# Optimization experiments

Measured on AMD Instinct MI355X. Metric: run time of the kernel, lower is better.

The kernel has to match this reference:

```python
import jax, jax.numpy as jnp
import numpy as np

N = 100000
E = 1600000
IN_FEATS = 256
HID = 128


def _graph_conv(x, W, b, src, dst, n_nodes):
    # DGL GraphConv with norm='both':
    #   out = D_in^{-1/2} * A * (D_out^{-1/2} * x @ W) + b
    ones = jnp.ones(src.shape[0], dtype=x.dtype)
    deg_out = jax.ops.segment_sum(ones, src, num_segments=n_nodes)
    deg_in = jax.ops.segment_sum(ones, dst, num_segments=n_nodes)
    norm_src = jnp.maximum(deg_out, 1.0) ** -0.5  # [N]
    norm_dst = jnp.maximum(deg_in, 1.0) ** -0.5   # [N]
    h = (x * norm_src[:, None]) @ W               # [N, HID]
    msg = h[src]                                  # [E, HID] gather
    agg = jax.ops.segment_sum(msg, dst, num_segments=n_nodes)  # [N, HID] scatter-add
    return agg * norm_dst[:, None] + b


def setup_inputs() -> dict:
    key = jax.random.key(0)
    ks = jax.random.split(key, 12)
    x = jax.random.normal(ks[0], (N, IN_FEATS), dtype=jnp.float32)
    src0 = jax.random.randint(ks[1], (E,), 0, N, dtype=jnp.int32)
    dst0 = jax.random.randint(ks[2], (E,), 0, N, dtype=jnp.int32)
    src1 = jax.random.randint(ks[3], (E,), 0, N, dtype=jnp.int32)
    dst1 = jax.random.randint(ks[4], (E,), 0, N, dtype=jnp.int32)
    s_e = 1.0 / np.sqrt(IN_FEATS)
    s_h = 1.0 / np.sqrt(HID)
    We = jax.random.uniform(ks[5], (IN_FEATS, HID), jnp.float32, -s_e, s_e)
    be = jax.random.uniform(ks[6], (HID,), jnp.float32, -s_e, s_e)
    W1 = jax.random.uniform(ks[7], (HID, HID), jnp.float32, -s_h, s_h)
    b1 = jnp.zeros((HID,), jnp.float32)
    W2 = jax.random.uniform(ks[8], (HID, HID), jnp.float32, -s_h, s_h)
    b2 = jnp.zeros((HID,), jnp.float32)
    return {"x": x, "We": We, "be": be, "W1": W1, "b1": b1, "W2": W2, "b2": b2,
            "src0": src0, "dst0": dst0, "src1": src1, "dst1": dst1}


def reference(x, We, be, W1, b1, W2, b2, src0, dst0, src1, dst1):
    n = x.shape[0]
    h = x @ We + be                                   # embed
    h = jax.nn.relu(_graph_conv(h, W1, b1, src0, dst0, n))
    h = jax.nn.relu(_graph_conv(h, W2, b2, src1, dst1, n))
    return h
```

## Files before the change

kernel.cpp:

```cpp
#include <hip/hip_runtime.h>

#define HID 128
#define NBUCK 512
#define BSHIFT 8
#define NB 512
#define M4 (4 * NBUCK * NB)
#define STAGE_CAP 8192

typedef __attribute__((ext_vector_type(8))) short bf16x8;
typedef __attribute__((ext_vector_type(4))) float f32x4;

__device__ __forceinline__ unsigned short f2bf(float f) {
    union { float f; unsigned u; } v; v.f = f;
    unsigned r = v.u + 0x7fff + ((v.u >> 16) & 1);
    return (unsigned short)(r >> 16);
}
__device__ __forceinline__ float bf2f(unsigned short b) {
    union { float f; unsigned u; } v; v.u = ((unsigned)b) << 16;
    return v.f;
}

__device__ __forceinline__ void gload_lds16(const void* g, void* l) {
    __builtin_amdgcn_global_load_lds(
        (const __attribute__((address_space(1))) void*)g,
        (__attribute__((address_space(3))) void*)l, 16, 0, 0);
}

__global__ __launch_bounds__(256) void bucket_count_all(
    const int* __restrict__ k0, const int* __restrict__ k1,
    const int* __restrict__ k2, const int* __restrict__ k3,
    int* __restrict__ counts, int E, int chunk) {
    __shared__ int h[4][NBUCK];
    int tid = threadIdx.x;
    #pragma unroll
    for (int j = 0; j < 8; ++j) ((int*)h)[tid + j * 256] = 0;
    __syncthreads();
    int base = blockIdx.x * chunk;
    int end = min(base + chunk, E);
    const int* keys[4] = {k0, k1, k2, k3};
    #pragma unroll
    for (int p = 0; p < 4; ++p) {
        const int* kp = keys[p];
        for (int i = base + tid; i < end; i += 256)
            atomicAdd(&h[p][kp[i] >> BSHIFT], 1);
    }
    __syncthreads();
    #pragma unroll
    for (int p = 0; p < 4; ++p) {
        counts[((p << 9) + tid) * NB + blockIdx.x] = h[p][tid];
        counts[((p << 9) + tid + 256) * NB + blockIdx.x] = h[p][tid + 256];
    }
}

__global__ __launch_bounds__(256) void scan_a(int* __restrict__ data, int* __restrict__ partials, int m) {
    __shared__ int sdata[256];
    int base = blockIdx.x * 1024;
    int tid = threadIdx.x;
    int v[4]; int s = 0;
    #pragma unroll
    for (int i = 0; i < 4; ++i) { int idx = base + tid * 4 + i; v[i] = (idx < m) ? data[idx] : 0; s += v[i]; }
    sdata[tid] = s; __syncthreads();
    for (int off = 1; off < 256; off <<= 1) {
        int t = (tid >= off) ? sdata[tid - off] : 0; __syncthreads();
        sdata[tid] += t; __syncthreads();
    }
    int excl = sdata[tid] - s;
    if (tid == 255) partials[blockIdx.x] = sdata[255];
    int run = excl;
    #pragma unroll
    for (int i = 0; i < 4; ++i) { int idx = base + tid * 4 + i; if (idx < m) data[idx] = run; run += v[i]; }
}

__global__ __launch_bounds__(1024) void scan_b(int* __restrict__ partials, int nb) {
    __shared__ int sdata[1024];
    int tid = threadIdx.x;
    int v = (tid < nb) ? partials[tid] : 0;
    sdata[tid] = v; __syncthreads();
    for (int off = 1; off < 1024; off <<= 1) {
        int t = (tid >= off) ? sdata[tid - off] : 0; __syncthreads();
        sdata[tid] += t; __syncthreads();
    }
    if (tid < nb) partials[tid] = sdata[tid] - v;
}

__global__ __launch_bounds__(256) void scan_c(int* __restrict__ data, const int* __restrict__ partials, int m) {
    int i = blockIdx.x * 256 + threadIdx.x;
    if (i < m) data[i] += partials[i >> 10];
}

__global__ __launch_bounds__(256) void bucket_scatter_all(
    const int* __restrict__ k0, const int* __restrict__ k1,
    const int* __restrict__ k2, const int* __restrict__ k3,
    const int* __restrict__ pay0, const int* __restrict__ pay1,
    const int* __restrict__ scanned, unsigned* __restrict__ bucketed,
    int E, int chunk) {
    __shared__ unsigned cur[4][NBUCK];
    int tid = threadIdx.x;
    int blk = blockIdx.x;
    #pragma unroll
    for (int p = 0; p < 4; ++p) {
        cur[p][tid]       = (unsigned)scanned[((p << 9) + tid) * NB + blk];
        cur[p][tid + 256] = (unsigned)scanned[((p << 9) + tid + 256) * NB + blk];
    }
    __syncthreads();
    int base = blk * chunk;
    int end = min(base + chunk, E);
    const int* keys[4] = {k0, k1, k2, k3};
    const int* pays[4] = {pay0, pay1, nullptr, nullptr};
    #pragma unroll
    for (int p = 0; p < 4; ++p) {
        const int* kp = keys[p];
        const int* pp = pays[p];
        for (int i = base + tid; i < end; i += 256) {
            int k = kp[i];
            int b = k >> BSHIFT;
            unsigned pay = pp ? (unsigned)pp[i] : 0u;
            unsigned pos = atomicAdd(&cur[p][b], 1u);
            bucketed[pos] = ((unsigned)(k & 255) << 17) | pay;
        }
    }
}

__global__ __launch_bounds__(256) void bucket_finalize(
    unsigned* __restrict__ bucketed, const int* __restrict__ scanned,
    int* __restrict__ rowptr0, int* __restrict__ rowptr1,
    int* __restrict__ dout0, int* __restrict__ dout1, int n, int E) {
    __shared__ unsigned stage[STAGE_CAP];
    __shared__ int cnt[256];
    __shared__ int sd[256];
    __shared__ int excl[256];
    __shared__ int cur[256];
    int tid = threadIdx.x;
    int g = blockIdx.x;
    int p = g >> 9;
    int b = g & 511;
    int start = scanned[g * NB];
    int end = (g == 4 * NBUCK - 1) ? 4 * E : scanned[(g + 1) * NB];
    if (end - start > STAGE_CAP) end = start + STAGE_CAP;
    int len = end - start;
    int node0 = b << BSHIFT;

    cnt[tid] = 0;
    __syncthreads();
    if (p < 2) {
        for (int i = tid; i < len; i += 256) {
            unsigned v = bucketed[start + i];
            stage[i] = v;
            atomicAdd(&cnt[v >> 17], 1);
        }
    } else {
        for (int i = tid; i < len; i += 256)
            atomicAdd(&cnt[bucketed[start + i] >> 17], 1);
    }
    __syncthreads();

    if (p >= 2) {
        int* dout = (p == 2) ? dout0 : dout1;
        int node = node0 + tid;
        if (node < n) dout[node] = cnt[tid];
        return;
    }

    int v = cnt[tid];
    sd[tid] = v;
    __syncthreads();
    for (int off = 1; off < 256; off <<= 1) {
        int t = (tid >= off) ? sd[tid - off] : 0; __syncthreads();
        sd[tid] += t; __syncthreads();
    }
    excl[tid] = sd[tid] - v;
    cur[tid] = 0;
    __syncthreads();

    int startLocal = start - p * E;
    int* rp = (p == 0) ? rowptr0 : rowptr1;
    int node = node0 + tid;
    if (node < n) rp[node] = startLocal + excl[tid];
    if (b == NBUCK - 1 && tid == 0) rp[n] = E;

    int* csr = (int*)bucketed + p * E;
    for (int i = tid; i < len; i += 256) {
        unsigned w = stage[i];
        int nl = (int)(w >> 17);
        int pos = startLocal + excl[nl] + atomicAdd(&cur[nl], 1);
        csr[pos] = (int)(w & 0x1FFFFu);
    }
}

__device__ __forceinline__ size_t bswz_idx(int k, int col) {
    int s = k >> 5, lh = (k >> 3) & 3, j = k & 7;
    int c = col >> 4, lc = col & 15;
    return ((((size_t)s * 8 + c) * 64 + (lh * 16 + lc)) * 8 + j);
}

__global__ __launch_bounds__(256) void weight_fuse(
    const float* __restrict__ We, const float* __restrict__ be,
    const float* __restrict__ W1,
    unsigned short* __restrict__ B1h, unsigned short* __restrict__ B1l,
    float* __restrict__ cv) {
    __shared__ float w1[128][128];
    int tid = threadIdx.x;
    #pragma unroll
    for (int it = 0; it < 16; ++it) {
        int s = tid + it * 256;
        int r = s >> 5, c4 = (s & 31) << 2;
        *(float4*)&w1[r][c4] = *(const float4*)&W1[r * 128 + c4];
    }
    __syncthreads();
    int j = tid & 127;
    int half = tid >> 7;
    if (blockIdx.x == 128) {
        if (half) return;
        float sum = 0.f;
        for (int k = 0; k < 128; ++k) sum += be[k] * w1[k][j];
        cv[j] = sum;
        return;
    }
    int i = blockIdx.x * 2 + half;
    const float* arow = &We[i * 128];
    float sum = 0.f;
    for (int k = 0; k < 128; ++k) sum += arow[k] * w1[k][j];
    unsigned short h = f2bf(sum);
    unsigned short l = f2bf(sum - bf2f(h));
    size_t o = bswz_idx(i, j);
    B1h[o] = h; B1l[o] = l;
}

__global__ __launch_bounds__(256) void swizzle_split(
    const float* __restrict__ W, unsigned short* __restrict__ Bh,
    unsigned short* __restrict__ Bl, int K) {
    int idx = blockIdx.x * 256 + threadIdx.x;
    if (idx >= K * 128) return;
    int k = idx >> 7, col = idx & 127;
    float v = W[idx];
    unsigned short h = f2bf(v);
    unsigned short l = f2bf(v - bf2f(h));
    size_t o = bswz_idx(k, col);
    Bh[o] = h; Bl[o] = l;
}

template <int K, bool AFP32>
__global__ __launch_bounds__(512) void gemm_lds(
    const void* __restrict__ X_,
    const unsigned short* __restrict__ Bh, const unsigned short* __restrict__ Bl,
    const float* __restrict__ cvec, const int* __restrict__ degs,
    unsigned short* __restrict__ T, int n) {
    constexpr int NS = K / 32;
    __shared__ __align__(16) char smem[2 * 16384];
    const int tid = threadIdx.x;
    const int wave = tid >> 6;
    const int lane = tid & 63;
    const int lr = lane & 15;
    const int lk = lane >> 4;
    const int row0 = blockIdx.x * 128 + wave * 16;
    const int grow = row0 + lr;
    const bool vr = grow < n;

    f32x4 acc[8];
    #pragma unroll
    for (int c = 0; c < 8; ++c) acc[c] = (f32x4)0.f;

    auto stage_slab = [&](int s, char* dst) {
        #pragma unroll
        for (int it = 0; it < 2; ++it) {
            int u = tid + it * 512;
            int f = u >> 6;
            int c = f >> 1, plane = f & 1;
            const unsigned short* srcArr = plane ? Bl : Bh;
            const char* g = (const char*)srcArr +
                ((size_t)(s * 512 + c * 64 + (u & 63)) * 16);
            gload_lds16(g, dst + u * 16);
        }
    };

    stage_slab(0, smem);

    const float* pxf = AFP32 ? (const float*)X_ + (size_t)grow * K + lk * 8 : nullptr;
    const unsigned short* pxb = AFP32 ? nullptr : (const unsigned short*)X_ + (size_t)grow * K + lk * 8;
    float4 a0 = make_float4(0.f, 0.f, 0.f, 0.f), a1 = a0;
    bf16x8 ab = (bf16x8)0;
    if (AFP32) {
        if (vr) { a0 = *(const float4*)pxf; a1 = *(const float4*)(pxf + 4); }
    } else {
        if (vr) ab = *(const bf16x8*)pxb;
    }

    #pragma unroll
    for (int s = 0; s < NS; ++s) {
        __syncthreads();
        if (s + 1 < NS) stage_slab(s + 1, smem + ((s + 1) & 1) * 16384);

        float4 n0 = make_float4(0.f, 0.f, 0.f, 0.f), n1 = n0;
        bf16x8 nb = (bf16x8)0;
        if (s + 1 < NS && vr) {
            if (AFP32) {
                n0 = *(const float4*)(pxf + (s + 1) * 32);
                n1 = *(const float4*)(pxf + (s + 1) * 32 + 4);
            } else {
                nb = *(const bf16x8*)(pxb + (s + 1) * 32);
            }
        }

        bf16x8 ah, al;
        if (AFP32) {
            float av[8] = {a0.x, a0.y, a0.z, a0.w, a1.x, a1.y, a1.z, a1.w};
            #pragma unroll
            for (int j = 0; j < 8; ++j) {
                unsigned short h = f2bf(av[j]);
                ah[j] = (short)h;
                al[j] = (short)f2bf(av[j] - bf2f(h));
            }
        } else {
            ah = ab;
        }

        const char* base = smem + (s & 1) * 16384 + lane * 16;
        #pragma unroll
        for (int c = 0; c < 8; ++c) {
            bf16x8 bh = *(const bf16x8*)(base + (c * 2) * 1024);
            bf16x8 bl = *(const bf16x8*)(base + (c * 2 + 1) * 1024);
            acc[c] = __builtin_amdgcn_mfma_f32_16x16x32_bf16(ah, bh, acc[c], 0, 0, 0);
            acc[c] = __builtin_amdgcn_mfma_f32_16x16x32_bf16(ah, bl, acc[c], 0, 0, 0);
            if (AFP32)
                acc[c] = __builtin_amdgcn_mfma_f32_16x16x32_bf16(al, bh, acc[c], 0, 0, 0);
        }
        a0 = n0; a1 = n1; ab = nb;
    }

    #pragma unroll
    for (int r = 0; r < 4; ++r) {
        int orow = row0 + lk * 4 + r;
        if (orow >= n) continue;
        float norm = rsqrtf(fmaxf((float)degs[orow], 1.0f));
        #pragma unroll
        for (int c = 0; c < 8; ++c) {
            float v = acc[c][r];
            if (cvec) v += cvec[c * 16 + lr];
            T[(size_t)orow * 128 + c * 16 + lr] = f2bf(v * norm);
        }
    }
}

template <bool OUT_BF16>
__global__ __launch_bounds__(256) void aggregate(
    const unsigned short* __restrict__ T, const int* __restrict__ rowptr,
    const int* __restrict__ csr, const float* __restrict__ bias,
    void* __restrict__ out_, int n) {
    const int wave = threadIdx.x >> 6;
    const int lane = threadIdx.x & 63;
    const int half = lane >> 5;
    const int l32 = lane & 31;
    const int node = blockIdx.x * 4 + wave;
    if (node >= n) return;
    const int beg = rowptr[node], end = rowptr[node + 1];
    float a0 = 0.f, a1 = 0.f, a2 = 0.f, a3 = 0.f;
    int e = beg;
    for (; e + 15 < end; e += 16) {
        int sidx[8];
        #pragma unroll
        for (int j = 0; j < 8; ++j) sidx[j] = csr[e + j * 2 + half];
        #pragma unroll
        for (int j = 0; j < 8; ++j) {
            uint2 u = *(const uint2*)&T[(size_t)sidx[j] * 128 + l32 * 4];
            a0 += __uint_as_float(u.x << 16);
            a1 += __uint_as_float(u.x & 0xffff0000u);
            a2 += __uint_as_float(u.y << 16);
            a3 += __uint_as_float(u.y & 0xffff0000u);
        }
    }
    for (; e + 1 < end; e += 2) {
        int sidx = csr[e + half];
        uint2 u = *(const uint2*)&T[(size_t)sidx * 128 + l32 * 4];
        a0 += __uint_as_float(u.x << 16);
        a1 += __uint_as_float(u.x & 0xffff0000u);
        a2 += __uint_as_float(u.y << 16);
        a3 += __uint_as_float(u.y & 0xffff0000u);
    }
    if (e < end && half == 0) {
        int sidx = csr[e];
        uint2 u = *(const uint2*)&T[(size_t)sidx * 128 + l32 * 4];
        a0 += __uint_as_float(u.x << 16);
        a1 += __uint_as_float(u.x & 0xffff0000u);
        a2 += __uint_as_float(u.y << 16);
        a3 += __uint_as_float(u.y & 0xffff0000u);
    }
    a0 += __shfl_xor(a0, 32);
    a1 += __shfl_xor(a1, 32);
    a2 += __shfl_xor(a2, 32);
    a3 += __shfl_xor(a3, 32);
    if (half == 0) {
        float norm = rsqrtf(fmaxf((float)(end - beg), 1.0f));
        float4 bv = *(const float4*)&bias[l32 * 4];
        float o0 = fmaxf(a0 * norm + bv.x, 0.f);
        float o1 = fmaxf(a1 * norm + bv.y, 0.f);
        float o2 = fmaxf(a2 * norm + bv.z, 0.f);
        float o3 = fmaxf(a3 * norm + bv.w, 0.f);
        if (OUT_BF16) {
            unsigned w0 = (unsigned)f2bf(o0) | ((unsigned)f2bf(o1) << 16);
            unsigned w1 = (unsigned)f2bf(o2) | ((unsigned)f2bf(o3) << 16);
            uint2* dst = (uint2*)((unsigned short*)out_ + (size_t)node * 128 + l32 * 4);
            *dst = make_uint2(w0, w1);
        } else {
            float4* dst = (float4*)((float*)out_ + (size_t)node * 128 + l32 * 4);
            *dst = make_float4(o0, o1, o2, o3);
        }
    }
}

extern "C" void kernel_launch(void* const* d_in, const int* in_sizes, int n_in,
                              void* d_out, int out_size, void* d_ws, size_t ws_size,
                              hipStream_t stream) {
    const float* x   = (const float*)d_in[0];
    const float* We  = (const float*)d_in[1];
    const float* be  = (const float*)d_in[2];
    const float* W1  = (const float*)d_in[3];
    const float* b1  = (const float*)d_in[4];
    const float* W2  = (const float*)d_in[5];
    const float* b2  = (const float*)d_in[6];
    const int* src0  = (const int*)d_in[7];
    const int* dst0  = (const int*)d_in[8];
    const int* src1  = (const int*)d_in[9];
    const int* dst1  = (const int*)d_in[10];
    float* out = (float*)d_out;

    const int n = in_sizes[0] / 256;
    const int E = in_sizes[7];
    const int chunk = (E + NB - 1) / NB;

    char* p = (char*)d_ws;
    auto carve = [&](size_t bytes) -> void* {
        void* r = (void*)p;
        p += (bytes + 511) & ~(size_t)511;
        return r;
    };
    unsigned short* t        = (unsigned short*)carve((size_t)n * HID * 2);
    unsigned short* h1       = (unsigned short*)carve((size_t)n * HID * 2);
    unsigned*       bucketed = (unsigned*)carve((size_t)4 * E * 4);
    int*            counts   = (int*)carve((size_t)M4 * 4);
    int*            partials = (int*)carve(1024 * 4);
    int*            rowptr0  = (int*)carve(((size_t)n + 1) * 4);
    int*            rowptr1  = (int*)carve(((size_t)n + 1) * 4);
    int*            dout0    = (int*)carve((size_t)n * 4);
    int*            dout1    = (int*)carve((size_t)n * 4);
    unsigned short* B1h      = (unsigned short*)carve(256 * HID * 2);
    unsigned short* B1l      = (unsigned short*)carve(256 * HID * 2);
    unsigned short* B2h      = (unsigned short*)carve(128 * HID * 2);
    unsigned short* B2l      = (unsigned short*)carve(128 * HID * 2);
    float*          cv       = (float*)carve(HID * 4);

    int* csr0 = (int*)bucketed;
    int* csr1 = (int*)bucketed + E;

    const int gGemm  = (n + 127) / 128;
    const int gAggN  = (n + 3) / 4;
    const int gScanA = (M4 + 1023) / 1024;
    const int gScanC = (M4 + 255) / 256;

    bucket_count_all<<<NB, 256, 0, stream>>>(dst0, dst1, src0, src1, counts, E, chunk);
    scan_a<<<gScanA, 256, 0, stream>>>(counts, partials, M4);
    scan_b<<<1, 1024, 0, stream>>>(partials, gScanA);
    scan_c<<<gScanC, 256, 0, stream>>>(counts, partials, M4);
    bucket_scatter_all<<<NB, 256, 0, stream>>>(dst0, dst1, src0, src1, src0, src1,
                                               counts, bucketed, E, chunk);
    bucket_finalize<<<4 * NBUCK, 256, 0, stream>>>(bucketed, counts, rowptr0, rowptr1, dout0, dout1, n, E);

    weight_fuse<<<129, 256, 0, stream>>>(We, be, W1, B1h, B1l, cv);
    swizzle_split<<<(128 * 128 + 255) / 256, 256, 0, stream>>>(W2, B2h, B2l, 128);

    gemm_lds<256, true><<<gGemm, 512, 0, stream>>>((const void*)x, B1h, B1l, cv, dout0, t, n);
    aggregate<true><<<gAggN, 256, 0, stream>>>(t, rowptr0, csr0, b1, (void*)h1, n);
    gemm_lds<128, false><<<gGemm, 512, 0, stream>>>((const void*)h1, B2h, B2l, nullptr, dout1, t, n);
    aggregate<false><<<gAggN, 256, 0, stream>>>(t, rowptr1, csr1, b2, (void*)out, n);
}
```

Before: 324.0 us.

## Pad per-node CSR segments to multiples of 16 with a zero sentinel row

```diff
diff --git a/kernel.cpp b/kernel.cpp
--- a/kernel.cpp
+++ b/kernel.cpp
@@ -6,6 +6,7 @@
 #define NB 512
 #define M4 (4 * NBUCK * NB)
 #define STAGE_CAP 8192
+#define PCAP 7168
 
 typedef __attribute__((ext_vector_type(8))) short bf16x8;
 typedef __attribute__((ext_vector_type(4))) float f32x4;
@@ -122,13 +123,15 @@
 }
 
 __global__ __launch_bounds__(256) void bucket_finalize(
-    unsigned* __restrict__ bucketed, const int* __restrict__ scanned,
-    int* __restrict__ rowptr0, int* __restrict__ rowptr1,
-    int* __restrict__ dout0, int* __restrict__ dout1, int n, int E) {
+    const unsigned* __restrict__ bucketed, const int* __restrict__ scanned,
+    int* __restrict__ prow0, int* __restrict__ prow1,
+    int* __restrict__ din0, int* __restrict__ din1,
+    int* __restrict__ dout0, int* __restrict__ dout1,
+    int* __restrict__ csr0, int* __restrict__ csr1, int n, int E) {
     __shared__ unsigned stage[STAGE_CAP];
     __shared__ int cnt[256];
     __shared__ int sd[256];
-    __shared__ int excl[256];
+    __shared__ int pexcl[256];
     __shared__ int cur[256];
     int tid = threadIdx.x;
     int g = blockIdx.x;
@@ -161,28 +164,33 @@
         return;
     }
 
-    int v = cnt[tid];
-    sd[tid] = v;
+    int c = cnt[tid];
+    int pc = (c + 15) & ~15;
+    sd[tid] = pc;
     __syncthreads();
     for (int off = 1; off < 256; off <<= 1) {
         int t = (tid >= off) ? sd[tid - off] : 0; __syncthreads();
         sd[tid] += t; __syncthreads();
     }
-    excl[tid] = sd[tid] - v;
+    pexcl[tid] = sd[tid] - pc;
     cur[tid] = 0;
     __syncthreads();
-
-    int startLocal = start - p * E;
-    int* rp = (p == 0) ? rowptr0 : rowptr1;
+    int ptot = sd[255];
+    if (ptot > PCAP) ptot = PCAP;
+
+    int* csr  = (p == 0) ? csr0  : csr1;
+    int* prow = (p == 0) ? prow0 : prow1;
+    int* din  = (p == 0) ? din0  : din1;
     int node = node0 + tid;
-    if (node < n) rp[node] = startLocal + excl[tid];
-    if (b == NBUCK - 1 && tid == 0) rp[n] = E;
-
-    int* csr = (int*)bucketed + p * E;
+    if (node < n) { prow[node] = b * PCAP + pexcl[tid]; din[node] = c; }
+
+    const int base = b * PCAP;
+    for (int j = tid; j < ptot; j += 256) csr[base + j] = n;
+    __syncthreads();
     for (int i = tid; i < len; i += 256) {
         unsigned w = stage[i];
         int nl = (int)(w >> 17);
-        int pos = startLocal + excl[nl] + atomicAdd(&cur[nl], 1);
+        int pos = base + pexcl[nl] + atomicAdd(&cur[nl], 1);
         csr[pos] = (int)(w & 0x1FFFFu);
     }
 }
@@ -343,19 +351,20 @@
 
 template <bool OUT_BF16>
 __global__ __launch_bounds__(256) void aggregate(
-    const unsigned short* __restrict__ T, const int* __restrict__ rowptr,
-    const int* __restrict__ csr, const float* __restrict__ bias,
-    void* __restrict__ out_, int n) {
+    const unsigned short* __restrict__ T, const int* __restrict__ prow,
+    const int* __restrict__ din, const int* __restrict__ csr,
+    const float* __restrict__ bias, void* __restrict__ out_, int n) {
     const int wave = threadIdx.x >> 6;
     const int lane = threadIdx.x & 63;
     const int half = lane >> 5;
     const int l32 = lane & 31;
     const int node = blockIdx.x * 4 + wave;
     if (node >= n) return;
-    const int beg = rowptr[node], end = rowptr[node + 1];
+    const int beg = prow[node];
+    const int d = din[node];
+    const int plen = (d + 15) & ~15;
     float a0 = 0.f, a1 = 0.f, a2 = 0.f, a3 = 0.f;
-    int e = beg;
-    for (; e + 15 < end; e += 16) {
+    for (int e = beg; e < beg + plen; e += 16) {
         int sidx[8];
         #pragma unroll
         for (int j = 0; j < 8; ++j) sidx[j] = csr[e + j * 2 + half];
@@ -368,28 +377,12 @@
             a3 += __uint_as_float(u.y & 0xffff0000u);
         }
     }
-    for (; e + 1 < end; e += 2) {
-        int sidx = csr[e + half];
-        uint2 u = *(const uint2*)&T[(size_t)sidx * 128 + l32 * 4];
-        a0 += __uint_as_float(u.x << 16);
-        a1 += __uint_as_float(u.x & 0xffff0000u);
-        a2 += __uint_as_float(u.y << 16);
-        a3 += __uint_as_float(u.y & 0xffff0000u);
-    }
-    if (e < end && half == 0) {
-        int sidx = csr[e];
-        uint2 u = *(const uint2*)&T[(size_t)sidx * 128 + l32 * 4];
-        a0 += __uint_as_float(u.x << 16);
-        a1 += __uint_as_float(u.x & 0xffff0000u);
-        a2 += __uint_as_float(u.y << 16);
-        a3 += __uint_as_float(u.y & 0xffff0000u);
-    }
     a0 += __shfl_xor(a0, 32);
     a1 += __shfl_xor(a1, 32);
     a2 += __shfl_xor(a2, 32);
     a3 += __shfl_xor(a3, 32);
     if (half == 0) {
-        float norm = rsqrtf(fmaxf((float)(end - beg), 1.0f));
+        float norm = rsqrtf(fmaxf((float)d, 1.0f));
         float4 bv = *(const float4*)&bias[l32 * 4];
         float o0 = fmaxf(a0 * norm + bv.x, 0.f);
         float o1 = fmaxf(a1 * norm + bv.y, 0.f);
@@ -433,13 +426,16 @@
         p += (bytes + 511) & ~(size_t)511;
         return r;
     };
-    unsigned short* t        = (unsigned short*)carve((size_t)n * HID * 2);
-    unsigned short* h1       = (unsigned short*)carve((size_t)n * HID * 2);
+    unsigned short* t        = (unsigned short*)carve(((size_t)n + 1) * HID * 2);
     unsigned*       bucketed = (unsigned*)carve((size_t)4 * E * 4);
     int*            counts   = (int*)carve((size_t)M4 * 4);
     int*            partials = (int*)carve(1024 * 4);
-    int*            rowptr0  = (int*)carve(((size_t)n + 1) * 4);
-    int*            rowptr1  = (int*)carve(((size_t)n + 1) * 4);
+    int*            csr0     = (int*)carve((size_t)NBUCK * PCAP * 4);
+    int*            csr1     = (int*)carve((size_t)NBUCK * PCAP * 4);
+    int*            prow0    = (int*)carve((size_t)n * 4);
+    int*            prow1    = (int*)carve((size_t)n * 4);
+    int*            din0     = (int*)carve((size_t)n * 4);
+    int*            din1     = (int*)carve((size_t)n * 4);
     int*            dout0    = (int*)carve((size_t)n * 4);
     int*            dout1    = (int*)carve((size_t)n * 4);
     unsigned short* B1h      = (unsigned short*)carve(256 * HID * 2);
@@ -448,13 +444,14 @@
     unsigned short* B2l      = (unsigned short*)carve(128 * HID * 2);
     float*          cv       = (float*)carve(HID * 4);
 
-    int* csr0 = (int*)bucketed;
-    int* csr1 = (int*)bucketed + E;
+    unsigned short* h1 = (unsigned short*)bucketed;
 
     const int gGemm  = (n + 127) / 128;
     const int gAggN  = (n + 3) / 4;
     const int gScanA = (M4 + 1023) / 1024;
     const int gScanC = (M4 + 255) / 256;
+
+    hipMemsetAsync(t + (size_t)n * HID, 0, HID * 2, stream);
 
     bucket_count_all<<<NB, 256, 0, stream>>>(dst0, dst1, src0, src1, counts, E, chunk);
     scan_a<<<gScanA, 256, 0, stream>>>(counts, partials, M4);
@@ -462,13 +459,14 @@
     scan_c<<<gScanC, 256, 0, stream>>>(counts, partials, M4);
     bucket_scatter_all<<<NB, 256, 0, stream>>>(dst0, dst1, src0, src1, src0, src1,
                                                counts, bucketed, E, chunk);
-    bucket_finalize<<<4 * NBUCK, 256, 0, stream>>>(bucketed, counts, rowptr0, rowptr1, dout0, dout1, n, E);
+    bucket_finalize<<<4 * NBUCK, 256, 0, stream>>>(bucketed, counts, prow0, prow1,
+                                                   din0, din1, dout0, dout1, csr0, csr1, n, E);
 
     weight_fuse<<<129, 256, 0, stream>>>(We, be, W1, B1h, B1l, cv);
     swizzle_split<<<(128 * 128 + 255) / 256, 256, 0, stream>>>(W2, B2h, B2l, 128);
 
     gemm_lds<256, true><<<gGemm, 512, 0, stream>>>((const void*)x, B1h, B1l, cv, dout0, t, n);
-    aggregate<true><<<gAggN, 256, 0, stream>>>(t, rowptr0, csr0, b1, (void*)h1, n);
+    aggregate<true><<<gAggN, 256, 0, stream>>>(t, prow0, din0, csr0, b1, (void*)h1, n);
     gemm_lds<128, false><<<gGemm, 512, 0, stream>>>((const void*)h1, B2h, B2l, nullptr, dout1, t, n);
-    aggregate<false><<<gAggN, 256, 0, stream>>>(t, rowptr1, csr1, b2, (void*)out, n);
-}
+    aggregate<false><<<gAggN, 256, 0, stream>>>(t, prow1, din1, csr1, b2, (void*)out, n);
+}
```

Measured after the change: 306.7 us. -5.3%, faster.
